# Optimization experiments

Hardware: AMD Instinct MI355X
Metric: run time of the kernel (lower is better)

## Reference

```python
import jax, jax.numpy as jnp
import numpy as np

B, C, H, W = 8, 512, 32, 32


def setup_inputs() -> dict:
    key = jax.random.key(0)
    ks = jax.random.split(key, 7)
    s = 0.02  # typical conv init scale
    return {
        "x": jax.random.normal(ks[0], (B, C, H, W), dtype=jnp.float32),
        "Wq": jax.random.normal(ks[1], (C, C), dtype=jnp.float32) * s,
        "bq": jax.random.normal(ks[2], (C,), dtype=jnp.float32) * s,
        "Wk": jax.random.normal(ks[3], (C, C), dtype=jnp.float32) * s,
        "bk": jax.random.normal(ks[4], (C,), dtype=jnp.float32) * s,
        "W6": jax.random.normal(ks[5], (C, C), dtype=jnp.float32) * s,
        "b6": jax.random.normal(ks[6], (C,), dtype=jnp.float32) * s,
    }


def _gam(x, Wq, bq, Wk, bk, W6, b6):
    b, c, h, w = x.shape
    hw = h * w
    scale = 1.0 / (c ** 0.5)
    # 1x1 convs == per-pixel channel matmuls (torch conv weight [out,in,1,1])
    q = jnp.einsum('bchw,dc->bhwd', x, Wq) + bq          # [B,H,W,C]
    q = q.reshape(b * hw, c)                              # query rows
    k = jnp.einsum('bchw,dc->bdhw', x, Wk) + bk[None, :, None, None]
    k = jnp.transpose(k, (1, 0, 2, 3)).reshape(c, b * hw)  # [C, B*HW]
    xw = (q.astype(jnp.float32) @ k.astype(jnp.float32))   # [B*HW, B*HW]
    xw = xw.reshape(b * hw, b, hw)
    xw = jnp.max(xw, axis=-1)                              # max over keys' spatial dim
    xw = jnp.mean(xw, axis=-1)                             # mean over key images
    xw = xw.reshape(b, hw) * scale
    xw = jax.nn.softmax(xw, axis=-1).astype(x.dtype)
    xw = xw.reshape(b, 1, h, w)
    x5 = x * xw
    return jnp.einsum('bchw,dc->bdhw', x5, W6) + b6[None, :, None, None]


def reference(x, Wq, bq, Wk, bk, W6, b6):
    x_new = _gam(x, Wq, bq, Wk, bk, W6, b6)
    # prototype: mean over batch and spatial dims, keep channels
    x_proto = jnp.mean(x_new.astype(jnp.float32), axis=(0, 2, 3)).astype(x.dtype)
    return x * x_proto[None, :, None, None]
```

## Files before the change

kernel.cpp:

```cpp
#include <hip/hip_runtime.h>
#include <hip/hip_bf16.h>

typedef __bf16 bf16_t;
typedef __bf16 bf16x8 __attribute__((ext_vector_type(8)));
typedef __bf16 bf16x4 __attribute__((ext_vector_type(4)));
typedef float f32x4 __attribute__((ext_vector_type(4)));

#define B_   8
#define C_   512
#define HW_  1024
#define NPIX 8192

typedef __attribute__((address_space(3))) void lds_vp;
typedef const __attribute__((address_space(1))) void gbl_vp;
__device__ __forceinline__ void gload_lds16(const void* g, void* l) {
    __builtin_amdgcn_global_load_lds((gbl_vp*)g, (lds_vp*)l, 16, 0, 0);
}

__device__ __forceinline__ void stage128x64_swz(const bf16_t* __restrict__ g,
                                                bf16_t* lds, int tid) {
    int w64 = tid & ~63;
#pragma unroll
    for (int s = 0; s < 4; ++s) {
        int u = s * 256 + tid;
        int row = u >> 3;
        int kg = (u & 7) ^ (row & 7);
        const bf16_t* src = g + (size_t)row * 512 + kg * 8;
        gload_lds16((const void*)src, (void*)(lds + (size_t)(s * 256 + w64) * 8));
    }
}

__global__ void k_transpose(const float* __restrict__ x, bf16_t* __restrict__ xT,
                            const float* __restrict__ Wq, const float* __restrict__ Wk,
                            bf16_t* __restrict__ wq, bf16_t* __restrict__ wk) {
    __shared__ bf16_t tile[64 * 65];
    int p0 = blockIdx.x * 64, c0 = blockIdx.y * 64, b = blockIdx.z;
    int t = threadIdx.x;
    int widx = ((blockIdx.z * 8 + blockIdx.y) * 16 + blockIdx.x) * 256 + t;
    wq[widx] = (bf16_t)Wq[widx];
    wk[widx] = (bf16_t)Wk[widx];
#pragma unroll
    for (int s = 0; s < 4; ++s) {
        int u = s * 256 + t;
        int cr = u >> 4, pc = (u & 15) * 4;
        float4 v = *(const float4*)&x[((size_t)(b * C_ + c0 + cr)) * HW_ + p0 + pc];
        tile[cr * 65 + pc + 0] = (bf16_t)v.x;
        tile[cr * 65 + pc + 1] = (bf16_t)v.y;
        tile[cr * 65 + pc + 2] = (bf16_t)v.z;
        tile[cr * 65 + pc + 3] = (bf16_t)v.w;
    }
    __syncthreads();
#pragma unroll
    for (int s = 0; s < 4; ++s) {
        int u = s * 256 + t;
        int pr = u >> 4, cc = (u & 15) * 4;
        bf16x4 o;
        o[0] = tile[(cc + 0) * 65 + pr];
        o[1] = tile[(cc + 1) * 65 + pr];
        o[2] = tile[(cc + 2) * 65 + pr];
        o[3] = tile[(cc + 3) * 65 + pr];
        *(bf16x4*)&xT[((size_t)(b * HW_ + p0 + pr)) * C_ + c0 + cc] = o;
    }
}

__launch_bounds__(256, 2)
__global__ void k_gemm_qk(const bf16_t* __restrict__ xT,
                          const bf16_t* __restrict__ wq, const bf16_t* __restrict__ wk,
                          const float* __restrict__ bq, const float* __restrict__ bk,
                          bf16_t* __restrict__ qo, bf16_t* __restrict__ ko) {
    __shared__ __align__(16) bf16_t As[128 * 64];
    __shared__ __align__(16) bf16_t Bs[128 * 64];
    int bid = blockIdx.x;
    int mtile = bid >> 3;
    int nt = bid & 7;
    const bf16_t* wsel = (nt < 4) ? wq : wk;
    const float*  bsel = (nt < 4) ? bq : bk;
    bf16_t*       osel = (nt < 4) ? qo : ko;
    int nb = (nt & 3) * 128;
    int i0 = mtile * 128;
    int tid = threadIdx.x;
    int lane = tid & 63, w = tid >> 6;
    int wr = w >> 1, wc = w & 1, lr = lane & 15, lg = lane >> 4;
    int kswz = (lg ^ (lr & 7)) << 4;

    f32x4 acc[4][4];
#pragma unroll
    for (int mi = 0; mi < 4; ++mi)
#pragma unroll
        for (int ni = 0; ni < 4; ++ni)
#pragma unroll
            for (int r = 0; r < 4; ++r) acc[mi][ni][r] = 0.f;

    for (int kt = 0; kt < 8; ++kt) {
        int k0 = kt * 64;
        stage128x64_swz(xT + (size_t)i0 * 512 + k0, As, tid);
        stage128x64_swz(wsel + (size_t)nb * 512 + k0, Bs, tid);
        asm volatile("s_waitcnt vmcnt(0)" ::: "memory");
        __builtin_amdgcn_s_barrier();
#pragma unroll
        for (int kk = 0; kk < 2; ++kk) {
            bf16x8 af[4], bfr[4];
#pragma unroll
            for (int mi = 0; mi < 4; ++mi)
                af[mi] = *(const bf16x8*)((const char*)As +
                    (wr * 64 + mi * 16 + lr) * 128 + (kswz ^ (kk * 64)));
#pragma unroll
            for (int ni = 0; ni < 4; ++ni)
                bfr[ni] = *(const bf16x8*)((const char*)Bs +
                    (wc * 64 + ni * 16 + lr) * 128 + (kswz ^ (kk * 64)));
#pragma unroll
            for (int mi = 0; mi < 4; ++mi)
#pragma unroll
                for (int ni = 0; ni < 4; ++ni)
                    acc[mi][ni] = __builtin_amdgcn_mfma_f32_16x16x32_bf16(
                        af[mi], bfr[ni], acc[mi][ni], 0, 0, 0);
        }
        __builtin_amdgcn_s_barrier();
    }
#pragma unroll
    for (int ni = 0; ni < 4; ++ni) {
        int col = nb + wc * 64 + ni * 16 + lr;
        float bias = bsel[col];
#pragma unroll
        for (int mi = 0; mi < 4; ++mi) {
            int rowb = i0 + wr * 64 + mi * 16 + lg * 4;
#pragma unroll
            for (int r = 0; r < 4; ++r)
                osel[(size_t)(rowb + r) * 512 + col] = (bf16_t)(acc[mi][ni][r] + bias);
        }
    }
}


#define STAGE_A(RH, D, T)                                                          \
    gload_lds16((const void*)(q + srcA + (size_t)((RH) * 128) * 512 +              \
                              ((T) & 7) * 64),                                     \
                (void*)(ldsb + (RH) * 32768 + (D) * 16384 + ldw));                 \
    gload_lds16((const void*)(q + srcA + (size_t)((RH) * 128 + 64) * 512 +         \
                              ((T) & 7) * 64),                                     \
                (void*)(ldsb + (RH) * 32768 + (D) * 16384 + 8192 + ldw));

#define STAGE_B(RH, D, T)                                                          \
    gload_lds16((const void*)(kb + srcB +                                          \
                              (size_t)(((T) >> 3) * 256 + (RH) * 128) * 512 +      \
                              ((T) & 7) * 64),                                     \
                (void*)(ldsb + 65536 + (RH) * 32768 + (D) * 16384 + ldw));         \
    gload_lds16((const void*)(kb + srcB +                                          \
                              (size_t)(((T) >> 3) * 256 + (RH) * 128 + 64) * 512 + \
                              ((T) & 7) * 64),                                     \
                (void*)(ldsb + 65536 + (RH) * 32768 + (D) * 16384 + 8192 + ldw));

#define PHASE(D, KH, MH, STAGE_STMT, VM_STMT)                                      \
    {                                                                              \
        const char* Ab = ldsb + wr * 32768 + (D) * 16384;                          \
        const char* Bb = ldsb + 65536 + (wc >> 1) * 32768 + (D) * 16384;           \
        _Pragma("unroll")                                                          \
        for (int mi = 0; mi < 4; ++mi)                                             \
            af[mi] = *(const bf16x8*)(Ab + (aswz ^ ((KH) * 64)) +                  \
                                      ((MH) * 4 + mi) * 2048);                     \
        if ((MH) == 0) {                                                           \
            _Pragma("unroll")                                                      \
            for (int ni = 0; ni < 4; ++ni)                                         \
                bf[ni] = *(const bf16x8*)(Bb + (bswz ^ ((KH) * 64)) + ni * 2048);  \
        }                                                                          \
        STAGE_STMT;                                                                \
        __builtin_amdgcn_s_setprio(1);                                             \
        _Pragma("unroll")                                                          \
        for (int mi = 0; mi < 4; ++mi)                                             \
            _Pragma("unroll")                                                      \
            for (int ni = 0; ni < 4; ++ni)                                         \
                acc[(MH) * 4 + mi][ni] = __builtin_amdgcn_mfma_f32_16x16x32_bf16(  \
                    af[mi], bf[ni], acc[(MH) * 4 + mi][ni], 0, 0, 0);              \
        __builtin_amdgcn_s_setprio(0);                                             \
        VM_STMT;                                                                   \
        __builtin_amdgcn_s_barrier();                                              \
    }

__global__ __launch_bounds__(512, 2)
void k_gemm_max8(const bf16_t* __restrict__ q, const bf16_t* __restrict__ kp,
                 float* __restrict__ Mout) {
    __shared__ __align__(16) bf16_t lds[65536];
    char* ldsb = (char*)lds;
    int bid = blockIdx.x;
    int img = bid & 7;
    int qp = bid >> 3;
    int i0 = qp * 256;
    const bf16_t* kb = kp + (size_t)img * HW_ * C_;
    int tid = threadIdx.x;
    int lane = tid & 63, w = tid >> 6;
    int wr = w >> 2, wc = w & 3;
    int lr = lane & 15, lg = lane >> 4;
    int kswz = (lg ^ (lr & 7)) << 4;
    int aswz = lr * 128 + kswz;
    int bswz = ((wc & 1) * 64 + lr) * 128 + kswz;

    int srow = tid >> 3;
    int sk = (((tid & 7) ^ ((tid >> 3) & 7))) << 3;
    size_t srcA = (size_t)(i0 + srow) * 512 + sk;
    size_t srcB = (size_t)srow * 512 + sk;
    int ldw = (tid >> 6) * 1024;

    f32x4 acc[8][4];
    bf16x8 af[4], bf[4];
    float rm[8][4];
#pragma unroll
    for (int mi = 0; mi < 8; ++mi)
#pragma unroll
        for (int ni = 0; ni < 4; ++ni)
#pragma unroll
            for (int r = 0; r < 4; ++r) acc[mi][ni][r] = 0.f;
#pragma unroll
    for (int mi = 0; mi < 8; ++mi)
#pragma unroll
        for (int r = 0; r < 4; ++r) rm[mi][r] = -3.4e38f;

    STAGE_B(0, 0, 0) STAGE_A(0, 0, 0) STAGE_B(1, 0, 0) STAGE_A(1, 0, 0)
    STAGE_B(0, 1, 1)
    asm volatile("s_waitcnt vmcnt(2)" ::: "memory");
    __builtin_amdgcn_s_barrier();

    for (int i = 0; i < 16; ++i) {
        int tb = 2 * i + 1, tc = 2 * i + 2, td = 2 * i + 3;
        bool s = (i < 15);
        PHASE(0, 0, 0, { STAGE_A(0, 1, tb) }, {})
        PHASE(0, 0, 1, { STAGE_B(1, 1, tb) }, {})
        PHASE(0, 1, 0, { STAGE_A(1, 1, tb) }, {})
        PHASE(0, 1, 1, { if (s) { STAGE_B(0, 0, tc) } },
              { if (s) { asm volatile("s_waitcnt vmcnt(2)" ::: "memory"); }
                else   { asm volatile("s_waitcnt vmcnt(0)" ::: "memory"); } })
        PHASE(1, 0, 0, { if (s) { STAGE_A(0, 0, tc) } }, {})
        PHASE(1, 0, 1, { if (s) { STAGE_B(1, 0, tc) } }, {})
        PHASE(1, 1, 0, { if (s) { STAGE_A(1, 0, tc) } }, {})
        PHASE(1, 1, 1, { if (s) { STAGE_B(0, 1, td) } },
              { if (s) { asm volatile("s_waitcnt vmcnt(2)" ::: "memory"); } })
        if ((i & 3) == 3) {
#pragma unroll
            for (int mi = 0; mi < 8; ++mi)
#pragma unroll
                for (int r = 0; r < 4; ++r) {
                    float v = fmaxf(fmaxf(acc[mi][0][r], acc[mi][1][r]),
                                    fmaxf(acc[mi][2][r], acc[mi][3][r]));
                    rm[mi][r] = fmaxf(rm[mi][r], v);
#pragma unroll
                    for (int ni = 0; ni < 4; ++ni) acc[mi][ni][r] = 0.f;
                }
        }
    }

#pragma unroll
    for (int mi = 0; mi < 8; ++mi)
#pragma unroll
        for (int r = 0; r < 4; ++r) {
            float v = rm[mi][r];
#pragma unroll
            for (int off = 1; off < 16; off <<= 1) v = fmaxf(v, __shfl_xor(v, off));
            rm[mi][r] = v;
        }
    float* sm = (float*)lds;
    if (lr == 0) {
#pragma unroll
        for (int mi = 0; mi < 8; ++mi)
#pragma unroll
            for (int r = 0; r < 4; ++r)
                sm[wc * 256 + wr * 128 + mi * 16 + lg * 4 + r] = rm[mi][r];
    }
    __syncthreads();
    if (tid < 256) {
        float v = fmaxf(fmaxf(sm[tid], sm[256 + tid]),
                        fmaxf(sm[512 + tid], sm[768 + tid]));
        Mout[(size_t)(i0 + tid) * 8 + img] = v;
    }
}

__global__ void k_softmax(const float* __restrict__ Mout, float* __restrict__ wsm) {
    int b = blockIdx.x;
    int t = threadIdx.x;
    __shared__ float red[16];
    const float scale = 0.044194173824159216f;
    float s[4];
#pragma unroll
    for (int i = 0; i < 4; ++i) {
        int p = t + i * 256;
        const float4* row = (const float4*)&Mout[(size_t)(b * 1024 + p) * 8];
        float4 r0 = row[0], r1 = row[1];
        float acc = (r0.x + r0.y + r0.z + r0.w) + (r1.x + r1.y + r1.z + r1.w);
        s[i] = acc * (scale / 8.0f);
    }
    float m = fmaxf(fmaxf(s[0], s[1]), fmaxf(s[2], s[3]));
#pragma unroll
    for (int off = 1; off < 64; off <<= 1) m = fmaxf(m, __shfl_xor(m, off));
    if ((t & 63) == 0) red[t >> 6] = m;
    __syncthreads();
    float m4 = fmaxf(fmaxf(red[0], red[1]), fmaxf(red[2], red[3]));
    float e[4], sum = 0.f;
#pragma unroll
    for (int i = 0; i < 4; ++i) { e[i] = __expf(s[i] - m4); sum += e[i]; }
#pragma unroll
    for (int off = 1; off < 64; off <<= 1) sum += __shfl_xor(sum, off);
    if ((t & 63) == 0) red[8 + (t >> 6)] = sum;
    __syncthreads();
    float tot = red[8] + red[9] + red[10] + red[11];
    float inv = 1.0f / tot;
#pragma unroll
    for (int i = 0; i < 4; ++i) wsm[b * 1024 + t + i * 256] = e[i] * inv;
}

__global__ void k_reduce_y(const float* __restrict__ x, const float* __restrict__ wsm,
                           float* __restrict__ y) {
    int c = blockIdx.x;
    int t = threadIdx.x;
    float acc = 0.f;
#pragma unroll
    for (int b = 0; b < 8; ++b) {
        float4 xv = ((const float4*)(x + ((size_t)(b * C_ + c)) * HW_))[t];
        float4 wv = ((const float4*)(wsm + b * HW_))[t];
        acc += xv.x * wv.x + xv.y * wv.y + xv.z * wv.z + xv.w * wv.w;
    }
#pragma unroll
    for (int off = 1; off < 64; off <<= 1) acc += __shfl_xor(acc, off);
    __shared__ float red[4];
    if ((t & 63) == 0) red[t >> 6] = acc;
    __syncthreads();
    if (t == 0) y[c] = (red[0] + red[1] + red[2] + red[3]) * (1.0f / 8192.0f);
}

__global__ void k_final(const float* __restrict__ x, const float* __restrict__ W6,
                        const float* __restrict__ b6, const float* __restrict__ y,
                        float* __restrict__ out) {
    int bid = blockIdx.x;
    int t = threadIdx.x;
    int c = bid & 511;
    float a = W6[(size_t)c * C_ + t] * y[t] +
              W6[(size_t)c * C_ + t + 256] * y[t + 256];
#pragma unroll
    for (int off = 1; off < 64; off <<= 1) a += __shfl_xor(a, off);
    __shared__ float red[4];
    if ((t & 63) == 0) red[t >> 6] = a;
    __syncthreads();
    float p = red[0] + red[1] + red[2] + red[3] + b6[c];
    int idx = bid * 256 + t;
    float4 v = ((const float4*)x)[idx];
    v.x *= p; v.y *= p; v.z *= p; v.w *= p;
    ((float4*)out)[idx] = v;
}

extern "C" void kernel_launch(void* const* d_in, const int* in_sizes, int n_in,
                              void* d_out, int out_size, void* d_ws, size_t ws_size,
                              hipStream_t stream) {
    const float* x  = (const float*)d_in[0];
    const float* Wq = (const float*)d_in[1];
    const float* bq = (const float*)d_in[2];
    const float* Wk = (const float*)d_in[3];
    const float* bk = (const float*)d_in[4];
    const float* W6 = (const float*)d_in[5];
    const float* b6 = (const float*)d_in[6];
    float* out = (float*)d_out;

    char* ws = (char*)d_ws;
    bf16_t* xT    = (bf16_t*)(ws);
    float*  Mout  = (float*)(ws);
    bf16_t* wqb   = (bf16_t*)(ws + 8388608);
    bf16_t* wkb   = (bf16_t*)(ws + 8912896);
    bf16_t* qb    = (bf16_t*)(ws + 9437184);
    bf16_t* kb    = (bf16_t*)(ws + 17825792);
    float*  wsm   = (float*)(ws + 26476544);
    float*  yv    = (float*)(ws + 26509312);

    hipLaunchKernelGGL(k_transpose, dim3(16, 8, 8), dim3(256), 0, stream,
                       x, xT, Wq, Wk, wqb, wkb);
    hipLaunchKernelGGL(k_gemm_qk, dim3(512), dim3(256), 0, stream,
                       xT, wqb, wkb, bq, bk, qb, kb);
    hipLaunchKernelGGL(k_gemm_max8, dim3(256), dim3(512), 0, stream, qb, kb, Mout);
    hipLaunchKernelGGL(k_softmax, dim3(8), dim3(256), 0, stream, Mout, wsm);
    hipLaunchKernelGGL(k_reduce_y, dim3(512), dim3(256), 0, stream, x, wsm, yv);
    hipLaunchKernelGGL(k_final, dim3(4096), dim3(256), 0, stream, x, W6, b6, yv, out);
}
```

Baseline: 95.16 us.

## Shrink QK-max GEMM tile to 128 rows with 4 waves and smaller LDS

Restructures the fused QK^T+max kernel. The block shrinks from 256 query rows and 8 waves to 128 rows and 4 waves, and the grid doubles to 512 blocks. LDS use drops to 48KB with a new K-half staging schedule and a narrower 32-element swizzle. The goal is more blocks per CU and better load balance across CUs. The cost is less reuse of each staged K tile and a tighter load/compute pipeline.

```diff
diff --git a/kernel.cpp b/kernel.cpp
--- a/kernel.cpp
+++ b/kernel.cpp
@@ -132,38 +132,36 @@
 }
 
 
-#define STAGE_A(RH, D, T)                                                          \
-    gload_lds16((const void*)(q + srcA + (size_t)((RH) * 128) * 512 +              \
-                              ((T) & 7) * 64),                                     \
-                (void*)(ldsb + (RH) * 32768 + (D) * 16384 + ldw));                 \
-    gload_lds16((const void*)(q + srcA + (size_t)((RH) * 128 + 64) * 512 +         \
-                              ((T) & 7) * 64),                                     \
-                (void*)(ldsb + (RH) * 32768 + (D) * 16384 + 8192 + ldw));
-
-#define STAGE_B(RH, D, T)                                                          \
+#define STAGE_A(KH, T)                                                             \
+    gload_lds16((const void*)(q + srcA + ((T) & 7) * 64 + (KH) * 32),              \
+                (void*)(ldsb + (KH) * 8192 + ldst));                               \
+    gload_lds16((const void*)(q + srcA + (size_t)64 * 512 + ((T) & 7) * 64 +       \
+                              (KH) * 32),                                          \
+                (void*)(ldsb + (KH) * 8192 + 4096 + ldst));
+
+#define STAGE_B(RH, KH, T)                                                         \
     gload_lds16((const void*)(kb + srcB +                                          \
                               (size_t)(((T) >> 3) * 256 + (RH) * 128) * 512 +      \
-                              ((T) & 7) * 64),                                     \
-                (void*)(ldsb + 65536 + (RH) * 32768 + (D) * 16384 + ldw));         \
+                              ((T) & 7) * 64 + (KH) * 32),                         \
+                (void*)(ldsb + 16384 + ((RH) * 2 + (KH)) * 8192 + ldst));          \
     gload_lds16((const void*)(kb + srcB +                                          \
                               (size_t)(((T) >> 3) * 256 + (RH) * 128 + 64) * 512 + \
-                              ((T) & 7) * 64),                                     \
-                (void*)(ldsb + 65536 + (RH) * 32768 + (D) * 16384 + 8192 + ldw));
-
-#define PHASE(D, KH, MH, STAGE_STMT, VM_STMT)                                      \
+                              ((T) & 7) * 64 + (KH) * 32),                         \
+                (void*)(ldsb + 16384 + ((RH) * 2 + (KH)) * 8192 + 4096 + ldst));
+
+#define PHASE(KH, MH, STG, VM)                                                     \
     {                                                                              \
-        const char* Ab = ldsb + wr * 32768 + (D) * 16384;                          \
-        const char* Bb = ldsb + 65536 + (wc >> 1) * 32768 + (D) * 16384;           \
+        const char* Ab = ldsb + (KH) * 8192;                                       \
         _Pragma("unroll")                                                          \
         for (int mi = 0; mi < 4; ++mi)                                             \
-            af[mi] = *(const bf16x8*)(Ab + (aswz ^ ((KH) * 64)) +                  \
-                                      ((MH) * 4 + mi) * 2048);                     \
+            af[mi] = *(const bf16x8*)(Ab + aswz + (MH) * 4096 + mi * 1024);        \
         if ((MH) == 0) {                                                           \
+            const char* Bb = ldsb + 16384 + ((wc >> 1) * 2 + (KH)) * 8192;         \
             _Pragma("unroll")                                                      \
             for (int ni = 0; ni < 4; ++ni)                                         \
-                bf[ni] = *(const bf16x8*)(Bb + (bswz ^ ((KH) * 64)) + ni * 2048);  \
+                bf[ni] = *(const bf16x8*)(Bb + bswz + ni * 1024);                  \
         }                                                                          \
-        STAGE_STMT;                                                                \
+        STG;                                                                       \
         __builtin_amdgcn_s_setprio(1);                                             \
         _Pragma("unroll")                                                          \
         for (int mi = 0; mi < 4; ++mi)                                             \
@@ -172,33 +170,32 @@
                 acc[(MH) * 4 + mi][ni] = __builtin_amdgcn_mfma_f32_16x16x32_bf16(  \
                     af[mi], bf[ni], acc[(MH) * 4 + mi][ni], 0, 0, 0);              \
         __builtin_amdgcn_s_setprio(0);                                             \
-        VM_STMT;                                                                   \
+        VM;                                                                        \
         __builtin_amdgcn_s_barrier();                                              \
     }
 
-__global__ __launch_bounds__(512, 2)
+__global__ __launch_bounds__(256, 2)
 void k_gemm_max8(const bf16_t* __restrict__ q, const bf16_t* __restrict__ kp,
                  float* __restrict__ Mout) {
-    __shared__ __align__(16) bf16_t lds[65536];
+    __shared__ __align__(16) bf16_t lds[24576];
     char* ldsb = (char*)lds;
     int bid = blockIdx.x;
     int img = bid & 7;
     int qp = bid >> 3;
-    int i0 = qp * 256;
+    int i0 = qp * 128;
     const bf16_t* kb = kp + (size_t)img * HW_ * C_;
     int tid = threadIdx.x;
     int lane = tid & 63, w = tid >> 6;
-    int wr = w >> 2, wc = w & 3;
+    int wc = w;
     int lr = lane & 15, lg = lane >> 4;
-    int kswz = (lg ^ (lr & 7)) << 4;
-    int aswz = lr * 128 + kswz;
-    int bswz = ((wc & 1) * 64 + lr) * 128 + kswz;
-
-    int srow = tid >> 3;
-    int sk = (((tid & 7) ^ ((tid >> 3) & 7))) << 3;
-    size_t srcA = (size_t)(i0 + srow) * 512 + sk;
-    size_t srcB = (size_t)srow * 512 + sk;
-    int ldw = (tid >> 6) * 1024;
+    int kswz = (lg ^ ((lr >> 1) & 3)) << 4;
+    int aswz = lr * 64 + kswz;
+    int bswz = ((wc & 1) * 64 + lr) * 64 + kswz;
+
+    int kg = (tid & 3) ^ ((tid >> 3) & 3);
+    size_t srcA = (size_t)(i0 + (tid >> 2)) * 512 + kg * 8;
+    size_t srcB = (size_t)(tid >> 2) * 512 + kg * 8;
+    int ldst = (tid & ~63) * 16;
 
     f32x4 acc[8][4];
     bf16x8 af[4], bf[4];
@@ -214,26 +211,23 @@
 #pragma unroll
         for (int r = 0; r < 4; ++r) rm[mi][r] = -3.4e38f;
 
-    STAGE_B(0, 0, 0) STAGE_A(0, 0, 0) STAGE_B(1, 0, 0) STAGE_A(1, 0, 0)
-    STAGE_B(0, 1, 1)
-    asm volatile("s_waitcnt vmcnt(2)" ::: "memory");
+    STAGE_B(0, 0, 0) STAGE_B(1, 0, 0)
+    STAGE_A(0, 0)
+    STAGE_B(0, 1, 0) STAGE_B(1, 1, 0)
+    asm volatile("s_waitcnt vmcnt(4)" ::: "memory");
     __builtin_amdgcn_s_barrier();
 
-    for (int i = 0; i < 16; ++i) {
-        int tb = 2 * i + 1, tc = 2 * i + 2, td = 2 * i + 3;
-        bool s = (i < 15);
-        PHASE(0, 0, 0, { STAGE_A(0, 1, tb) }, {})
-        PHASE(0, 0, 1, { STAGE_B(1, 1, tb) }, {})
-        PHASE(0, 1, 0, { STAGE_A(1, 1, tb) }, {})
-        PHASE(0, 1, 1, { if (s) { STAGE_B(0, 0, tc) } },
-              { if (s) { asm volatile("s_waitcnt vmcnt(2)" ::: "memory"); }
+    for (int T = 0; T < 32; ++T) {
+        bool s = (T < 31);
+        int Tn = T + 1;
+        PHASE(0, 0, { STAGE_A(1, T) }, {})
+        PHASE(0, 1, { if (s) { STAGE_B(0, 0, Tn) STAGE_B(1, 0, Tn) } },
+              { if (s) { asm volatile("s_waitcnt vmcnt(4)" ::: "memory"); }
                 else   { asm volatile("s_waitcnt vmcnt(0)" ::: "memory"); } })
-        PHASE(1, 0, 0, { if (s) { STAGE_A(0, 0, tc) } }, {})
-        PHASE(1, 0, 1, { if (s) { STAGE_B(1, 0, tc) } }, {})
-        PHASE(1, 1, 0, { if (s) { STAGE_A(1, 0, tc) } }, {})
-        PHASE(1, 1, 1, { if (s) { STAGE_B(0, 1, td) } },
-              { if (s) { asm volatile("s_waitcnt vmcnt(2)" ::: "memory"); } })
-        if ((i & 3) == 3) {
+        PHASE(1, 0, { if (s) { STAGE_A(0, Tn) } }, {})
+        PHASE(1, 1, { if (s) { STAGE_B(0, 1, Tn) STAGE_B(1, 1, Tn) } },
+              { if (s) { asm volatile("s_waitcnt vmcnt(4)" ::: "memory"); } })
+        if ((T & 7) == 7) {
 #pragma unroll
             for (int mi = 0; mi < 8; ++mi)
 #pragma unroll
@@ -262,12 +256,12 @@
         for (int mi = 0; mi < 8; ++mi)
 #pragma unroll
             for (int r = 0; r < 4; ++r)
-                sm[wc * 256 + wr * 128 + mi * 16 + lg * 4 + r] = rm[mi][r];
-    }
-    __syncthreads();
-    if (tid < 256) {
-        float v = fmaxf(fmaxf(sm[tid], sm[256 + tid]),
-                        fmaxf(sm[512 + tid], sm[768 + tid]));
+                sm[wc * 128 + mi * 16 + lg * 4 + r] = rm[mi][r];
+    }
+    __syncthreads();
+    if (tid < 128) {
+        float v = fmaxf(fmaxf(sm[tid], sm[128 + tid]),
+                        fmaxf(sm[256 + tid], sm[384 + tid]));
         Mout[(size_t)(i0 + tid) * 8 + img] = v;
     }
 }
@@ -370,7 +364,7 @@
                        x, xT, Wq, Wk, wqb, wkb);
     hipLaunchKernelGGL(k_gemm_qk, dim3(512), dim3(256), 0, stream,
                        xT, wqb, wkb, bq, bk, qb, kb);
-    hipLaunchKernelGGL(k_gemm_max8, dim3(256), dim3(512), 0, stream, qb, kb, Mout);
+    hipLaunchKernelGGL(k_gemm_max8, dim3(512), dim3(256), 0, stream, qb, kb, Mout);
     hipLaunchKernelGGL(k_softmax, dim3(8), dim3(256), 0, stream, Mout, wsm);
     hipLaunchKernelGGL(k_reduce_y, dim3(512), dim3(256), 0, stream, x, wsm, yv);
     hipLaunchKernelGGL(k_final, dim3(4096), dim3(256), 0, stream, x, W6, b6, yv, out);
```

Measured after the change: 104.7 us. 10.0% more time.
